# Kernel tuning notes

Hardware: AMD Instinct MI355X
Metric: run time of the kernel (lower is better)

Reference implementation:

```python
import jax, jax.numpy as jnp
import numpy as np

N = 32          # agents_num
IN_DIM = 16     # node feature dim (excluding 2 pos cols)
HID = 128
HEADS = 4
OUT = 5
DUEL_H = 256
RADIUS = 0.3
LATENT = HID + HID * HEADS * 2  # 1152
BS = 128


def _lin(k, i, o):
    s = 1.0 / np.sqrt(i)
    return jax.random.uniform(k, (i, o), minval=-s, maxval=s, dtype=jnp.float32)


def setup_inputs() -> dict:
    key = jax.random.key(0)
    ks = jax.random.split(key, 16)
    pos = jax.random.uniform(ks[0], (BS, N, 2))
    feats = jax.random.normal(ks[1], (BS, N, IN_DIM))
    aidx = jax.random.randint(ks[2], (BS,), 0, N).astype(jnp.float32)
    node = jnp.concatenate([pos, feats], axis=-1).reshape(BS, N * (2 + IN_DIM))
    obs = jnp.concatenate([node, aidx[:, None]], axis=1)  # (BS, N*(2+IN_DIM)+1)
    return {
        "obs": obs,
        "enc_w1": _lin(ks[3], IN_DIM, HID), "enc_b1": jnp.zeros((HID,)),
        "enc_w2": _lin(ks[4], HID, HID), "enc_b2": jnp.zeros((HID,)),
        "wl1": _lin(ks[5], HID, HEADS * HID), "wr1": _lin(ks[6], HID, HEADS * HID),
        "att1": jax.random.normal(ks[7], (HEADS, HID)) * 0.1, "bias1": jnp.zeros((HEADS * HID,)),
        "wl2": _lin(ks[8], HID * HEADS, HEADS * HID), "wr2": _lin(ks[9], HID * HEADS, HEADS * HID),
        "att2": jax.random.normal(ks[10], (HEADS, HID)) * 0.1, "bias2": jnp.zeros((HEADS * HID,)),
        "q_w1": _lin(ks[11], LATENT, DUEL_H), "q_b1": jnp.zeros((DUEL_H,)),
        "q_w2": _lin(ks[12], DUEL_H, OUT), "q_b2": jnp.zeros((OUT,)),
        "v_w1": _lin(ks[13], LATENT, DUEL_H), "v_b1": jnp.zeros((DUEL_H,)),
        "v_w2": _lin(ks[14], DUEL_H, 1), "v_b2": jnp.zeros((1,)),
    }


def _gatv2(x, adj, wl, wr, att, bias):
    # Dense-masked GATv2 (PyG semantics: lin_l on source j, lin_r on target i,
    # leaky_relu(x_i + x_j) . att, softmax over neighbors j, aggregate lin_l(x_j)).
    bs, n, _ = x.shape
    gl = (x @ wl).reshape(bs, n, HEADS, HID)  # source transform
    gr = (x @ wr).reshape(bs, n, HEADS, HID)  # target transform
    e = jax.nn.leaky_relu(gr[:, :, None] + gl[:, None, :], 0.2)  # [b, i, j, h, c]
    logits = jnp.einsum('bijhc,hc->bijh', e, att)
    logits = jnp.where(adj[..., None], logits, -jnp.inf)  # diag always True (self loops)
    alpha = jax.nn.softmax(logits, axis=2)
    out = jnp.einsum('bijh,bjhc->bihc', alpha, gl).reshape(bs, n, HEADS * HID)
    return out + bias


def reference(obs, enc_w1, enc_b1, enc_w2, enc_b2,
              wl1, wr1, att1, bias1, wl2, wr2, att2, bias2,
              q_w1, q_b1, q_w2, q_b2, v_w1, v_b1, v_w2, v_b2):
    bs = obs.shape[0]
    node = obs[:, :-1].reshape(bs, N, 2 + IN_DIM)
    pos, feats = node[..., :2], node[..., 2:]
    aidx = jnp.clip(obs[:, -1], 0, N - 1).astype(jnp.int32)

    # radius_graph (per-graph, loop=False) + GATv2 add_self_loops => diag True
    d2 = jnp.sum((pos[:, :, None] - pos[:, None, :]) ** 2, axis=-1)  # [bs, N, N]
    adj = (d2 < RADIUS ** 2) | jnp.eye(N, dtype=bool)

    # encoder MLP then ReLU (as in forward)
    h = jax.nn.relu(feats @ enc_w1 + enc_b1)
    x = jax.nn.relu(h @ enc_w2 + enc_b2)  # [bs, N, HID]

    b = jnp.arange(bs)
    x1 = x[b, aidx]  # [bs, HID]

    x = jax.nn.relu(_gatv2(x, adj, wl1, wr1, att1, bias1))  # [bs, N, HID*HEADS]
    x2 = x[b, aidx]

    x = jax.nn.relu(_gatv2(x, adj, wl2, wr2, att2, bias2))
    x3 = x[b, aidx]

    x_cat = jnp.concatenate([x1, x2, x3], axis=1)  # [bs, LATENT]

    q = jax.nn.relu(x_cat @ q_w1 + q_b1) @ q_w2 + q_b2  # [bs, OUT]
    v = jax.nn.relu(x_cat @ v_w1 + v_b1) @ v_w2 + v_b2  # [bs, 1]
    return q - q.mean(axis=1, keepdims=True) + v
```

## Files before the change

### kernel.cpp

```cpp
#include <hip/hip_runtime.h>
#include <hip/hip_bf16.h>

typedef unsigned int uint_t;
typedef unsigned short ushort_t;
typedef __attribute__((ext_vector_type(8))) short short8;
typedef __attribute__((ext_vector_type(4))) float floatx4;

__device__ __forceinline__ float4 fma4(float4 a, float s, float4 w){
  a.x += s*w.x; a.y += s*w.y; a.z += s*w.z; a.w += s*w.w; return a;
}
__device__ __forceinline__ float4 relu4(float4 a){
  return make_float4(fmaxf(a.x,0.f),fmaxf(a.y,0.f),fmaxf(a.z,0.f),fmaxf(a.w,0.f));
}
__device__ __forceinline__ unsigned bf16rne(float f){
  unsigned u = __float_as_uint(f);
  return (u + 0x7fffu + ((u>>16)&1u)) >> 16;
}
__device__ __forceinline__ uint_t packbf(float f){
  unsigned hb = bf16rne(f);
  float hf = __uint_as_float(hb<<16);
  unsigned lb = bf16rne(f - hf);
  return (hb<<16) | lb;
}
__device__ __forceinline__ uint4 pack4(float4 v){
  uint4 u; u.x=packbf(v.x); u.y=packbf(v.y); u.z=packbf(v.z); u.w=packbf(v.w); return u;
}
__device__ __forceinline__ float unpk(uint_t u){
  return __uint_as_float(u & 0xffff0000u) + __uint_as_float(u<<16);
}
#define UNPACK8(u0,u1,hi,lo) \
  hi[0]=(short)(u0.x>>16); lo[0]=(short)u0.x; \
  hi[1]=(short)(u0.y>>16); lo[1]=(short)u0.y; \
  hi[2]=(short)(u0.z>>16); lo[2]=(short)u0.z; \
  hi[3]=(short)(u0.w>>16); lo[3]=(short)u0.w; \
  hi[4]=(short)(u1.x>>16); lo[4]=(short)u1.x; \
  hi[5]=(short)(u1.y>>16); lo[5]=(short)u1.y; \
  hi[6]=(short)(u1.z>>16); lo[6]=(short)u1.z; \
  hi[7]=(short)(u1.w>>16); lo[7]=(short)u1.w;


template<int NKC>
__device__ __forceinline__ void hgemm_body(
    const uint_t* __restrict__ xcatpk,
    const ushort_t* __restrict__ qw1Thi, const ushort_t* __restrict__ qw1Tlo,
    const ushort_t* __restrict__ vw1Thi, const ushort_t* __restrict__ vw1Tlo,
    float* __restrict__ part, int ks, int ct, int t, int k0c, int slot0)
{
  const int w = t>>6, lane = t&63, m = lane&15, quad = lane>>4;
  const ushort_t* Bhi = (ct<4) ? qw1Thi : vw1Thi;
  const int cbl = (ct<4) ? ct*64 : (ct-4)*64;
  const int cbg = (ct<4) ? ct*64 : 256 + (ct-4)*64;
  const int kb = k0c + ks*NKC;
  const uint_t* ap = xcatpk + (size_t)w*18432 + m*32 + quad*8 + (size_t)kb*512;
  const ushort_t* bp0 = Bhi + (size_t)((cbl>>4)+0)*18432 + m*32 + quad*8 + (size_t)kb*512;
  const ushort_t* bp1 = Bhi + (size_t)((cbl>>4)+1)*18432 + m*32 + quad*8 + (size_t)kb*512;
  const ushort_t* bp2 = Bhi + (size_t)((cbl>>4)+2)*18432 + m*32 + quad*8 + (size_t)kb*512;
  const ushort_t* bp3 = Bhi + (size_t)((cbl>>4)+3)*18432 + m*32 + quad*8 + (size_t)kb*512;
  const size_t lod = (size_t)(qw1Tlo - qw1Thi);
  floatx4 acc[4];
  #pragma unroll
  for (int i=0;i<4;i++) acc[i] = (floatx4){0.f,0.f,0.f,0.f};
  #pragma unroll
  for (int kc=0; kc<NKC; kc++){
    const uint4 ua0 = *(const uint4*)(ap);
    const uint4 ua1 = *(const uint4*)(ap+4);
    ap += 512;
    short8 ahi, alo;
    UNPACK8(ua0,ua1,ahi,alo)
    const ushort_t* bps[4] = {bp0, bp1, bp2, bp3};
    #pragma unroll
    for (int nt=0; nt<4; nt++){
      const short8 bh = *(const short8*)(bps[nt] + kc*512);
      const short8 bl = *(const short8*)(bps[nt] + kc*512 + lod);
      acc[nt] = __builtin_amdgcn_mfma_f32_16x16x32_bf16(ahi, bh, acc[nt], 0,0,0);
      acc[nt] = __builtin_amdgcn_mfma_f32_16x16x32_bf16(ahi, bl, acc[nt], 0,0,0);
      acc[nt] = __builtin_amdgcn_mfma_f32_16x16x32_bf16(alo, bh, acc[nt], 0,0,0);
    }
  }
  float* pdst = part + (size_t)(slot0+ks)*65536;
  const int crow0 = w*16 + quad*4;
  #pragma unroll
  for (int nt=0; nt<4; nt++){
    const int col = cbg + nt*16 + m;
    #pragma unroll
    for (int r=0;r<4;r++)
      pdst[(size_t)(crow0 + r)*512 + col] = acc[nt][r];
  }
}

__global__ __launch_bounds__(256) void prep_kernel(
    const float* __restrict__ obs,
    const float* __restrict__ enc_w1, const float* __restrict__ enc_b1,
    const float* __restrict__ enc_w2, const float* __restrict__ enc_b2,
    const float* __restrict__ wl1, const float* __restrict__ wr1,
    ushort_t* __restrict__ wl1Thi, ushort_t* __restrict__ wl1Tlo,
    ushort_t* __restrict__ wr1Thi, ushort_t* __restrict__ wr1Tlo,
    uint_t* __restrict__ xpk, uint_t* __restrict__ xcatpk,
    unsigned* __restrict__ adjw, int* __restrict__ aiw)
{
  const int t = threadIdx.x, bid = blockIdx.x;
  if (bid >= 512){
    __shared__ float sm[32][33];
    const int cw = bid - 512;
    const float* in; ushort_t* ohi; ushort_t* olo; int tt;
    const int K = 128, N = 512;
    if (cw < 64){ in=wl1; ohi=wl1Thi; olo=wl1Tlo; tt=cw; }
    else        { in=wr1; ohi=wr1Thi; olo=wr1Tlo; tt=cw-64; }
    const int ktiles = K>>5;
    const int kt = tt % ktiles, nt = tt / ktiles;
    const int r = t>>5, c = t&31;
    #pragma unroll
    for (int i=0;i<4;i++)
      sm[r+i*8][c] = in[(size_t)(kt*32 + r + i*8)*N + nt*32 + c];
    __syncthreads();
    #pragma unroll
    for (int i=0;i<4;i++){
      const int nl = r + i*8;
      const int n  = nt*32 + nl;
      const float f = sm[c][nl];
      const unsigned hb = bf16rne(f);
      const float hf = __uint_as_float(hb<<16);
      const unsigned lb = bf16rne(f - hf);
      const size_t off = (size_t)(n>>4)*(16*K) + (size_t)kt*512 + (size_t)(n&15)*32 + c;
      ohi[off] = (ushort_t)hb;
      olo[off] = (ushort_t)lb;
    }
    return;
  }
  __shared__ float s_pos[64];
  __shared__ float s_feats[128];
  __shared__ __align__(16) float s_h[8*132];
  __shared__ int s_ai;
  const int s = bid & 127, g = bid >> 7;
  const float* ob = obs + s*577;

  if (t==0){
    float a = ob[576];
    a = fminf(fmaxf(a, 0.f), 31.f);
    s_ai = (int)a;
    if (g==0) aiw[s] = (int)a;
  }
  if (t < 128){ const int n=t>>4, f=t&15; s_feats[t] = ob[(g*8+n)*18+2+f]; }
  if (g==0 && t>=128 && t<192){ const int u=t-128; s_pos[u] = ob[(u>>1)*18 + (u&1)]; }
  __syncthreads();

  if (g==0 && t < 32){
    const float px = s_pos[2*t], py = s_pos[2*t+1];
    const float R2 = 0.09f;
    unsigned mm = 0u;
    for (int j=0;j<32;j++){
      const float dx = __fsub_rn(px, s_pos[2*j]), dy = __fsub_rn(py, s_pos[2*j+1]);
      const float d2 = __fadd_rn(__fmul_rn(dx,dx), __fmul_rn(dy,dy));
      if (d2 <= R2 || j==t) mm |= (1u<<j);
    }
    adjw[s*32+t] = mm;
  }

  const int n = t>>5, c0 = (t&31)*4;
  {
    float4 a = *(const float4*)(enc_b1+c0);
    #pragma unroll
    for (int f=0; f<16; f++)
      a = fma4(a, s_feats[n*16+f], *(const float4*)(enc_w1 + f*128 + c0));
    *(float4*)&s_h[n*132+c0] = relu4(a);
  }
  __syncthreads();
  {
    float4 a = *(const float4*)(enc_b2+c0);
    for (int k=0;k<128;k+=4){
      const float4 hv = *(const float4*)&s_h[n*132+k];
      a = fma4(a, hv.x, *(const float4*)(enc_w2 + (k+0)*128 + c0));
      a = fma4(a, hv.y, *(const float4*)(enc_w2 + (k+1)*128 + c0));
      a = fma4(a, hv.z, *(const float4*)(enc_w2 + (k+2)*128 + c0));
      a = fma4(a, hv.w, *(const float4*)(enc_w2 + (k+3)*128 + c0));
    }
    a = relu4(a);
    const uint4 p = pack4(a);
    const int i = g*8 + n;
    uint_t* xp = xpk + (size_t)(s*2 + (i>>4))*2048 + (c0>>5)*512 + (i&15)*32 + (c0&31);
    *(uint4*)xp = p;
    if (i == s_ai){
      uint_t* xc = xcatpk + (size_t)(s>>4)*18432 + (c0>>5)*512 + (s&15)*32 + (c0&31);
      *(uint4*)xc = p;
    }
  }
}

__global__ __launch_bounds__(512) void pa1_kernel(
    const uint_t* __restrict__ xpk,
    const ushort_t* __restrict__ wl1Thi, const ushort_t* __restrict__ wl1Tlo,
    const ushort_t* __restrict__ wr1Thi, const ushort_t* __restrict__ wr1Tlo,
    const float* __restrict__ att, const float* __restrict__ bias,
    const unsigned* __restrict__ adjw, const int* __restrict__ aiw,
    const float* __restrict__ wl2, const float* __restrict__ q_w1,
    const float* __restrict__ v_w1, const float* __restrict__ wr2,
    ushort_t* __restrict__ wl2Thi, ushort_t* __restrict__ wl2Tlo,
    ushort_t* __restrict__ qw1Thi, ushort_t* __restrict__ qw1Tlo,
    ushort_t* __restrict__ vw1Thi, ushort_t* __restrict__ vw1Tlo,
    ushort_t* __restrict__ wr2Thi, ushort_t* __restrict__ wr2Tlo,
    uint_t* __restrict__ x2pk, uint_t* __restrict__ xcatpk)
{
  __shared__ __align__(16) float s_gl[32*132];
  __shared__ __align__(16) float s_gr[32*132];
  __shared__ __align__(16) float s_att[128];
  __shared__ __align__(16) float s_b[128];
  __shared__ float s_lg[32*33];
  __shared__ unsigned s_adj[32];
  const int t = threadIdx.x, bid = blockIdx.x;

  if (bid >= 512){
    const int cw = bid - 512;
    const float* in; ushort_t* ohi; ushort_t* olo; int K, N, tt;
    if (cw < 256)      { in=wl2;  ohi=wl2Thi; olo=wl2Tlo; K=512;  N=512; tt=cw; }
    else if (cw < 544) { in=q_w1; ohi=qw1Thi; olo=qw1Tlo; K=1152; N=256; tt=cw-256; }
    else if (cw < 832) { in=v_w1; ohi=vw1Thi; olo=vw1Tlo; K=1152; N=256; tt=cw-544; }
    else               { in=wr2;  ohi=wr2Thi; olo=wr2Tlo; K=512;  N=512; tt=cw-832; }
    const int ktiles = K>>5;
    const int kt = tt % ktiles, nt = tt / ktiles;
    const int r = t>>5, c = t&31;
    #pragma unroll
    for (int i=0;i<2;i++)
      s_gl[(r+i*16)*33 + c] = in[(size_t)(kt*32 + r + i*16)*N + nt*32 + c];
    __syncthreads();
    #pragma unroll
    for (int i=0;i<2;i++){
      const int nl = r + i*16;
      const int n  = nt*32 + nl;
      const float f = s_gl[c*33 + nl];
      const unsigned hb = bf16rne(f);
      const float hf = __uint_as_float(hb<<16);
      const unsigned lb = bf16rne(f - hf);
      const size_t off = (size_t)(n>>4)*(16*K) + (size_t)kt*512 + (size_t)(n&15)*32 + c;
      ohi[off] = (ushort_t)hb;
      olo[off] = (ushort_t)lb;
    }
    return;
  }

  const int s = bid & 127, h = bid >> 7;
  const int w = t>>6, lane = t&63, m = lane&15, quad = lane>>4;
  const int mat = w>>2, cpair = w&3;

  if (t < 128){ s_att[t] = att[h*128 + t]; s_b[t] = bias[h*128 + t]; }
  if (t >= 224 && t < 256) s_adj[t-224] = adjw[s*32 + (t-224)];
  const int ai = aiw[s];

  const ushort_t* Bhi = (mat==0) ? wl1Thi : wr1Thi;
  const ushort_t* Blo = (mat==0) ? wl1Tlo : wr1Tlo;
  const int nbase = h*8 + cpair*2;
  const uint_t* a0p = xpk + (size_t)(s*2+0)*2048 + m*32 + quad*8;
  const uint_t* a1p = xpk + (size_t)(s*2+1)*2048 + m*32 + quad*8;
  const ushort_t* bp0 = Bhi + (size_t)(nbase+0)*2048 + m*32 + quad*8;
  const ushort_t* bp1 = Bhi + (size_t)(nbase+1)*2048 + m*32 + quad*8;
  const size_t lod = (size_t)(Blo - Bhi);
  floatx4 acc[2][2];
  #pragma unroll
  for (int i=0;i<2;i++)
    #pragma unroll
    for (int j=0;j<2;j++) acc[i][j] = (floatx4){0.f,0.f,0.f,0.f};

  #pragma unroll
  for (int kc=0; kc<4; kc++){
    const uint4 u00 = *(const uint4*)(a0p + kc*512);
    const uint4 u01 = *(const uint4*)(a0p + kc*512 + 4);
    const uint4 u10 = *(const uint4*)(a1p + kc*512);
    const uint4 u11 = *(const uint4*)(a1p + kc*512 + 4);
    short8 ahi0, alo0, ahi1, alo1;
    UNPACK8(u00,u01,ahi0,alo0)
    UNPACK8(u10,u11,ahi1,alo1)
    const ushort_t* bps[2] = {bp0, bp1};
    #pragma unroll
    for (int nt=0; nt<2; nt++){
      const short8 bh = *(const short8*)(bps[nt] + kc*512);
      const short8 bl = *(const short8*)(bps[nt] + kc*512 + lod);
      acc[0][nt] = __builtin_amdgcn_mfma_f32_16x16x32_bf16(ahi0, bh, acc[0][nt], 0,0,0);
      acc[0][nt] = __builtin_amdgcn_mfma_f32_16x16x32_bf16(ahi0, bl, acc[0][nt], 0,0,0);
      acc[0][nt] = __builtin_amdgcn_mfma_f32_16x16x32_bf16(alo0, bh, acc[0][nt], 0,0,0);
      acc[1][nt] = __builtin_amdgcn_mfma_f32_16x16x32_bf16(ahi1, bh, acc[1][nt], 0,0,0);
      acc[1][nt] = __builtin_amdgcn_mfma_f32_16x16x32_bf16(ahi1, bl, acc[1][nt], 0,0,0);
      acc[1][nt] = __builtin_amdgcn_mfma_f32_16x16x32_bf16(alo1, bh, acc[1][nt], 0,0,0);
    }
  }
  {
    float* dst = mat ? s_gr : s_gl;
    const int colbase = cpair*32;
    #pragma unroll
    for (int nt=0; nt<2; nt++){
      const int col = colbase + nt*16 + m;
      #pragma unroll
      for (int r=0;r<4;r++){
        dst[(quad*4+r)*132 + col]      = acc[0][nt][r];
        dst[(16+quad*4+r)*132 + col]   = acc[1][nt][r];
      }
    }
  }
  __syncthreads();

  {
    const int i = t>>4, jb = t&15;
    float lacc[2] = {0.f,0.f};
    for (int c=0;c<128;c+=4){
      const float4 g = *(const float4*)&s_gr[i*132+c];
      const float4 a = *(const float4*)&s_att[c];
      #pragma unroll
      for (int mm=0;mm<2;mm++){
        const float4 gj = *(const float4*)&s_gl[(jb+16*mm)*132 + c];
        float ex = g.x+gj.x; ex = fmaxf(ex, 0.2f*ex);
        float ey = g.y+gj.y; ey = fmaxf(ey, 0.2f*ey);
        float ez = g.z+gj.z; ez = fmaxf(ez, 0.2f*ez);
        float ew = g.w+gj.w; ew = fmaxf(ew, 0.2f*ew);
        lacc[mm] += ex*a.x + ey*a.y + ez*a.z + ew*a.w;
      }
    }
    s_lg[i*33 + jb]      = lacc[0];
    s_lg[i*33 + jb + 16] = lacc[1];
  }
  __syncthreads();

  #pragma unroll
  for (int rnd=0; rnd<2; rnd++){
    const int i = rnd*16 + (t>>5), j = t&31;
    const float lg = s_lg[i*33+j];
    const bool ok = (s_adj[i]>>j)&1u;
    float v = ok ? lg : -3.0e38f;
    #pragma unroll
    for (int d_=16; d_; d_>>=1) v = fmaxf(v, __shfl_xor(v, d_, 32));
    const float e = ok ? __expf(lg - v) : 0.f;
    float sum = e;
    #pragma unroll
    for (int d_=16; d_; d_>>=1) sum += __shfl_xor(sum, d_, 32);
    s_lg[i*33+j] = e / sum;
  }
  __syncthreads();

  {
    const int i = t>>4, c0 = (t&15)*8;
    float4 o0 = make_float4(0.f,0.f,0.f,0.f), o1 = o0;
    for (int j=0;j<32;j++){
      const float al = s_lg[i*33+j];
      o0 = fma4(o0, al, *(const float4*)&s_gl[j*132 + c0]);
      o1 = fma4(o1, al, *(const float4*)&s_gl[j*132 + c0 + 4]);
    }
    const float4 b0 = *(const float4*)&s_b[c0];
    const float4 b1 = *(const float4*)&s_b[c0+4];
    o0 = relu4(make_float4(o0.x+b0.x, o0.y+b0.y, o0.z+b0.z, o0.w+b0.w));
    o1 = relu4(make_float4(o1.x+b1.x, o1.y+b1.y, o1.z+b1.z, o1.w+b1.w));
    const uint4 p0 = pack4(o0), p1 = pack4(o1);
    const int kb = h*128 + c0;
    uint_t* xp = x2pk + (size_t)(s*2 + (i>>4))*8192 + (kb>>5)*512 + (i&15)*32 + (kb&31);
    *(uint4*)&xp[0] = p0;
    *(uint4*)&xp[4] = p1;
    if (i == ai){
      const int kk = 128 + kb;
      uint_t* tp = xcatpk + (size_t)(s>>4)*18432 + (kk>>5)*512 + (s&15)*32 + (kk&31);
      *(uint4*)&tp[0] = p0;
      *(uint4*)&tp[4] = p1;
    }
  }
}

__global__ __launch_bounds__(512) void gr2_kernel(
    const uint_t* __restrict__ xcatpk,
    const ushort_t* __restrict__ wr2Thi, const ushort_t* __restrict__ wr2Tlo,
    const ushort_t* __restrict__ qw1Thi, const ushort_t* __restrict__ qw1Tlo,
    const ushort_t* __restrict__ vw1Thi, const ushort_t* __restrict__ vw1Tlo,
    float* __restrict__ hpart, float* __restrict__ GR)
{
  const int t = threadIdx.x, bid = blockIdx.x;
  if (bid >= 32){
    const int hk = bid - 32;
    hgemm_body<5>(xcatpk, qw1Thi, qw1Tlo, vw1Thi, vw1Tlo, hpart, hk>>3, hk&7, t, 0, 0);
    return;
  }
  const int w = t>>6, lane = t&63, m = lane&15, quad = lane>>4;
  const int rt = w;
  const int ctl = bid;
  const uint_t* ap = xcatpk + (size_t)rt*18432 + m*32 + quad*8 + (size_t)4*512;
  const ushort_t* bp = wr2Thi + (size_t)ctl*8192 + m*32 + quad*8;
  const size_t lod = (size_t)(wr2Tlo - wr2Thi);
  floatx4 acc = (floatx4){0.f,0.f,0.f,0.f};
  #pragma unroll 4
  for (int kc=0; kc<16; kc++){
    const uint4 ua0 = *(const uint4*)(ap + kc*512);
    const uint4 ua1 = *(const uint4*)(ap + kc*512 + 4);
    short8 ahi, alo;
    UNPACK8(ua0,ua1,ahi,alo)
    const short8 bh = *(const short8*)(bp + kc*512);
    const short8 bl = *(const short8*)(bp + kc*512 + lod);
    acc = __builtin_amdgcn_mfma_f32_16x16x32_bf16(ahi, bh, acc, 0,0,0);
    acc = __builtin_amdgcn_mfma_f32_16x16x32_bf16(ahi, bl, acc, 0,0,0);
    acc = __builtin_amdgcn_mfma_f32_16x16x32_bf16(alo, bh, acc, 0,0,0);
  }
  const int row0 = rt*16 + quad*4, col = ctl*16 + m;
  #pragma unroll
  for (int r=0;r<4;r++)
    GR[(size_t)(row0 + r)*512 + col] = acc[r];
}

__global__ __launch_bounds__(512) void pa2_kernel(
    const uint_t* __restrict__ x2pk,
    const ushort_t* __restrict__ wl2Thi, const ushort_t* __restrict__ wl2Tlo,
    const float* __restrict__ GR,
    const float* __restrict__ att2, const float* __restrict__ bias2,
    const unsigned* __restrict__ adjw, const int* __restrict__ aiw,
    uint_t* __restrict__ xcatpk)
{
  __shared__ __align__(16) float s_gl[32*132];
  __shared__ __align__(16) float s_p2[128];
  __shared__ __align__(16) float s_at[128];
  __shared__ __align__(16) float s_bb[128];
  __shared__ float s_lg[32];
  __shared__ float s_al[32];
  const int t = threadIdx.x, bid = blockIdx.x;
  const int s = bid & 127, h = bid >> 7;
  const int w = t>>6, lane = t&63, m = lane&15, quad = lane>>4;
  const int ai = aiw[s];
  const unsigned arow = adjw[s*32+ai];

  if (t < 128){
    s_p2[t] = GR[(size_t)s*512 + h*128 + t];
    s_at[t] = att2[h*128+t];
    s_bb[t] = bias2[h*128+t];
  }

  const uint_t* a0p = x2pk + (size_t)(s*2+0)*8192 + m*32 + quad*8;
  const uint_t* a1p = x2pk + (size_t)(s*2+1)*8192 + m*32 + quad*8;
  const ushort_t* bq = wl2Thi + (size_t)(h*8 + w)*8192 + m*32 + quad*8;
  const size_t lod = (size_t)(wl2Tlo - wl2Thi);
  floatx4 acc0 = (floatx4){0.f,0.f,0.f,0.f}, acc1 = acc0;
  #pragma unroll 4
  for (int kc=0; kc<16; kc++){
    const uint4 u00 = *(const uint4*)(a0p + kc*512);
    const uint4 u01 = *(const uint4*)(a0p + kc*512 + 4);
    const uint4 u10 = *(const uint4*)(a1p + kc*512);
    const uint4 u11 = *(const uint4*)(a1p + kc*512 + 4);
    short8 ahi0, alo0, ahi1, alo1;
    UNPACK8(u00,u01,ahi0,alo0)
    UNPACK8(u10,u11,ahi1,alo1)
    const short8 bh = *(const short8*)(bq + kc*512);
    const short8 bl = *(const short8*)(bq + kc*512 + lod);
    acc0 = __builtin_amdgcn_mfma_f32_16x16x32_bf16(ahi0, bh, acc0, 0,0,0);
    acc0 = __builtin_amdgcn_mfma_f32_16x16x32_bf16(ahi0, bl, acc0, 0,0,0);
    acc0 = __builtin_amdgcn_mfma_f32_16x16x32_bf16(alo0, bh, acc0, 0,0,0);
    acc1 = __builtin_amdgcn_mfma_f32_16x16x32_bf16(ahi1, bh, acc1, 0,0,0);
    acc1 = __builtin_amdgcn_mfma_f32_16x16x32_bf16(ahi1, bl, acc1, 0,0,0);
    acc1 = __builtin_amdgcn_mfma_f32_16x16x32_bf16(alo1, bh, acc1, 0,0,0);
  }
  {
    const int col = w*16 + m;
    #pragma unroll
    for (int r=0;r<4;r++){
      s_gl[(quad*4+r)*132 + col]    = acc0[r];
      s_gl[(16+quad*4+r)*132 + col] = acc1[r];
    }
  }
  __syncthreads();

  if (t < 256){
    const int j = t>>3, pq = t&7;
    float sum = 0.f;
    #pragma unroll
    for (int q=0;q<4;q++){
      const int c = pq*16 + q*4;
      const float4 g = *(const float4*)&s_gl[j*132 + c];
      const float4 r = *(const float4*)&s_p2[c];
      const float4 a = *(const float4*)&s_at[c];
      float e0 = r.x+g.x; e0 = fmaxf(e0, 0.2f*e0);
      float e1 = r.y+g.y; e1 = fmaxf(e1, 0.2f*e1);
      float e2 = r.z+g.z; e2 = fmaxf(e2, 0.2f*e2);
      float e3 = r.w+g.w; e3 = fmaxf(e3, 0.2f*e3);
      sum += e0*a.x + e1*a.y + e2*a.z + e3*a.w;
    }
    sum += __shfl_xor(sum,1,64);
    sum += __shfl_xor(sum,2,64);
    sum += __shfl_xor(sum,4,64);
    if (pq==0) s_lg[j] = sum;
  }
  __syncthreads();
  if (t < 32){
    const float lg = s_lg[t];
    const bool ok = (arow>>t)&1u;
    float v = ok ? lg : -3.0e38f;
    #pragma unroll
    for (int d_=16; d_; d_>>=1) v = fmaxf(v, __shfl_xor(v, d_, 32));
    const float e = ok ? __expf(lg - v) : 0.f;
    float sm = e;
    #pragma unroll
    for (int d_=16; d_; d_>>=1) sm += __shfl_xor(sm, d_, 32);
    s_al[t] = e / sm;
  }
  __syncthreads();
  if (t < 128){
    float acc2 = 0.f;
    #pragma unroll 8
    for (int j=0;j<32;j++) acc2 += s_al[j] * s_gl[j*132 + t];
    const float x3v = fmaxf(acc2 + s_bb[t], 0.f);
    const int kk = 640 + h*128 + t;
    xcatpk[(size_t)(s>>4)*18432 + (kk>>5)*512 + (s&15)*32 + (kk&31)] = packbf(x3v);
  }
}

__global__ __launch_bounds__(512) void x3g_kernel(
    const uint_t* __restrict__ xcatpk,
    const ushort_t* __restrict__ qw1Thi, const ushort_t* __restrict__ qw1Tlo,
    const ushort_t* __restrict__ vw1Thi, const ushort_t* __restrict__ vw1Tlo,
    float* __restrict__ hpart)
{
  const int t = threadIdx.x, bid = blockIdx.x;
  hgemm_body<4>(xcatpk, qw1Thi, qw1Tlo, vw1Thi, vw1Tlo, hpart, bid>>3, bid&7, t, 20, 4);
}

__global__ __launch_bounds__(256) void hepi_kernel(
    const float* __restrict__ hpart,
    const float* __restrict__ q_b1, const float* __restrict__ q_w2, const float* __restrict__ q_b2,
    const float* __restrict__ v_b1, const float* __restrict__ v_w2, const float* __restrict__ v_b2,
    float* __restrict__ out)
{
  __shared__ float s_p[4*6];
  const int t = threadIdx.x, s = blockIdx.x;
  float hq = q_b1[t], hv = v_b1[t];
  #pragma unroll
  for (int ks=0; ks<8; ks++){
    hq += hpart[(size_t)ks*65536 + (size_t)s*512 + t];
    hv += hpart[(size_t)ks*65536 + (size_t)s*512 + 256 + t];
  }
  hq = fmaxf(hq, 0.f);
  hv = fmaxf(hv, 0.f);
  float p[6];
  #pragma unroll
  for (int o=0;o<5;o++) p[o] = hq * q_w2[t*5+o];
  p[5] = hv * v_w2[t];
  #pragma unroll
  for (int d_=32; d_; d_>>=1){
    #pragma unroll
    for (int o=0;o<6;o++) p[o] += __shfl_xor(p[o], d_, 64);
  }
  const int w = t>>6, lane = t&63;
  if (lane==0){
    #pragma unroll
    for (int o=0;o<6;o++) s_p[w*6+o] = p[o];
  }
  __syncthreads();
  if (t < 6) s_p[t] = s_p[t] + s_p[6+t] + s_p[12+t] + s_p[18+t];
  __syncthreads();
  if (t < 5){
    const float q0 = s_p[0]+q_b2[0], q1 = s_p[1]+q_b2[1], q2 = s_p[2]+q_b2[2],
                q3 = s_p[3]+q_b2[3], q4 = s_p[4]+q_b2[4];
    const float mean = (q0+q1+q2+q3+q4) / 5.0f;
    const float v = s_p[5] + v_b2[0];
    const float qt = (t==0?q0:t==1?q1:t==2?q2:t==3?q3:q4);
    out[s*5+t] = qt - mean + v;
  }
}

extern "C" void kernel_launch(void* const* d_in, const int* in_sizes, int n_in,
                              void* d_out, int out_size, void* d_ws, size_t ws_size,
                              hipStream_t stream) {
  (void)n_in; (void)out_size; (void)ws_size;
  const float* obs    = (const float*)d_in[0];
  const float* enc_w1 = (const float*)d_in[1];
  const float* enc_b1 = (const float*)d_in[2];
  const float* enc_w2 = (const float*)d_in[3];
  const float* enc_b2 = (const float*)d_in[4];
  const float* wl1    = (const float*)d_in[5];
  const float* wr1    = (const float*)d_in[6];
  const float* att1   = (const float*)d_in[7];
  const float* bias1  = (const float*)d_in[8];
  const float* wl2    = (const float*)d_in[9];
  const float* wr2    = (const float*)d_in[10];
  const float* att2   = (const float*)d_in[11];
  const float* bias2  = (const float*)d_in[12];
  const float* q_w1   = (const float*)d_in[13];
  const float* q_b1   = (const float*)d_in[14];
  const float* q_w2   = (const float*)d_in[15];
  const float* q_b2   = (const float*)d_in[16];
  const float* v_w1   = (const float*)d_in[17];
  const float* v_b1   = (const float*)d_in[18];
  const float* v_w2   = (const float*)d_in[19];
  const float* v_b2   = (const float*)d_in[20];

  char* ws = (char*)d_ws;
  uint_t*   x_pk    = (uint_t*)  (ws + 0);
  float*    hpart   = (float*)   (ws + 0);
  uint_t*   xcat_pk = (uint_t*)  (ws + 2097152);
  unsigned* adjw    = (unsigned*)(ws + 2686976);
  int*      aiw     = (int*)     (ws + 2703360);
  uint_t*   x2_pk   = (uint_t*)  (ws + 2703872);
  ushort_t* wl1Thi  = (ushort_t*)(ws + 11092480);
  ushort_t* wl1Tlo  = (ushort_t*)(ws + 11223552);
  ushort_t* wr1Thi  = (ushort_t*)(ws + 11354624);
  ushort_t* wr1Tlo  = (ushort_t*)(ws + 11485696);
  ushort_t* wl2Thi  = (ushort_t*)(ws + 11616768);
  ushort_t* wl2Tlo  = (ushort_t*)(ws + 12141056);
  ushort_t* qw1Thi  = (ushort_t*)(ws + 12665344);
  ushort_t* qw1Tlo  = (ushort_t*)(ws + 13255168);
  ushort_t* vw1Thi  = (ushort_t*)(ws + 13844992);
  ushort_t* vw1Tlo  = (ushort_t*)(ws + 14434816);
  ushort_t* wr2Thi  = (ushort_t*)(ws + 15024640);
  ushort_t* wr2Tlo  = (ushort_t*)(ws + 15548928);
  float*    GR      = (float*)   (ws + 16073216);

  const int bs = in_sizes[0] / 577;
  (void)bs;

  prep_kernel<<<512 + 128, 256, 0, stream>>>(obs, enc_w1, enc_b1, enc_w2, enc_b2,
      wl1, wr1, wl1Thi, wl1Tlo, wr1Thi, wr1Tlo,
      x_pk, xcat_pk, adjw, aiw);

  pa1_kernel<<<512 + 1088, 512, 0, stream>>>(x_pk, wl1Thi, wl1Tlo, wr1Thi, wr1Tlo,
      att1, bias1, adjw, aiw,
      wl2, q_w1, v_w1, wr2,
      wl2Thi, wl2Tlo, qw1Thi, qw1Tlo, vw1Thi, vw1Tlo, wr2Thi, wr2Tlo,
      x2_pk, xcat_pk);

  gr2_kernel<<<64, 512, 0, stream>>>(xcat_pk, wr2Thi, wr2Tlo,
      qw1Thi, qw1Tlo, vw1Thi, vw1Tlo, hpart, GR);

  pa2_kernel<<<512, 512, 0, stream>>>(x2_pk, wl2Thi, wl2Tlo, GR,
      att2, bias2, adjw, aiw, xcat_pk);

  x3g_kernel<<<32, 512, 0, stream>>>(xcat_pk, qw1Thi, qw1Tlo, vw1Thi, vw1Tlo, hpart);

  hepi_kernel<<<128, 256, 0, stream>>>(hpart, q_b1, q_w2, q_b2, v_b1, v_w2, v_b2,
                                       (float*)d_out);
}
```

Before: 197.0 us.

## Fuse second GAT layer and dueling head into one per-sample tail kernel

Replaces the gr2, pa2, x3g and hepi kernels with a single tail kernel, one block per sample. Each block gathers the agent rows, computes the wr2 target projection and the q/v first layers as plain fp32 GEMVs reading the original weights, and loops over the four heads for layer-2 attention. This drops three launches, the bf16 hi/lo transposes of q_w1, v_w1 and wr2, and the partial-sum round trips through global memory. In exchange, only 128 blocks run and the heads are processed one after another. Each block also re-reads several MB of fp32 weights with scalar FMA loops instead of MFMA, which could leave the tail latency- and bandwidth-bound.

```diff
diff --git a/kernel.cpp b/kernel.cpp
--- a/kernel.cpp
+++ b/kernel.cpp
@@ -39,55 +39,6 @@
   hi[7]=(short)(u1.w>>16); lo[7]=(short)u1.w;
 
 
-template<int NKC>
-__device__ __forceinline__ void hgemm_body(
-    const uint_t* __restrict__ xcatpk,
-    const ushort_t* __restrict__ qw1Thi, const ushort_t* __restrict__ qw1Tlo,
-    const ushort_t* __restrict__ vw1Thi, const ushort_t* __restrict__ vw1Tlo,
-    float* __restrict__ part, int ks, int ct, int t, int k0c, int slot0)
-{
-  const int w = t>>6, lane = t&63, m = lane&15, quad = lane>>4;
-  const ushort_t* Bhi = (ct<4) ? qw1Thi : vw1Thi;
-  const int cbl = (ct<4) ? ct*64 : (ct-4)*64;
-  const int cbg = (ct<4) ? ct*64 : 256 + (ct-4)*64;
-  const int kb = k0c + ks*NKC;
-  const uint_t* ap = xcatpk + (size_t)w*18432 + m*32 + quad*8 + (size_t)kb*512;
-  const ushort_t* bp0 = Bhi + (size_t)((cbl>>4)+0)*18432 + m*32 + quad*8 + (size_t)kb*512;
-  const ushort_t* bp1 = Bhi + (size_t)((cbl>>4)+1)*18432 + m*32 + quad*8 + (size_t)kb*512;
-  const ushort_t* bp2 = Bhi + (size_t)((cbl>>4)+2)*18432 + m*32 + quad*8 + (size_t)kb*512;
-  const ushort_t* bp3 = Bhi + (size_t)((cbl>>4)+3)*18432 + m*32 + quad*8 + (size_t)kb*512;
-  const size_t lod = (size_t)(qw1Tlo - qw1Thi);
-  floatx4 acc[4];
-  #pragma unroll
-  for (int i=0;i<4;i++) acc[i] = (floatx4){0.f,0.f,0.f,0.f};
-  #pragma unroll
-  for (int kc=0; kc<NKC; kc++){
-    const uint4 ua0 = *(const uint4*)(ap);
-    const uint4 ua1 = *(const uint4*)(ap+4);
-    ap += 512;
-    short8 ahi, alo;
-    UNPACK8(ua0,ua1,ahi,alo)
-    const ushort_t* bps[4] = {bp0, bp1, bp2, bp3};
-    #pragma unroll
-    for (int nt=0; nt<4; nt++){
-      const short8 bh = *(const short8*)(bps[nt] + kc*512);
-      const short8 bl = *(const short8*)(bps[nt] + kc*512 + lod);
-      acc[nt] = __builtin_amdgcn_mfma_f32_16x16x32_bf16(ahi, bh, acc[nt], 0,0,0);
-      acc[nt] = __builtin_amdgcn_mfma_f32_16x16x32_bf16(ahi, bl, acc[nt], 0,0,0);
-      acc[nt] = __builtin_amdgcn_mfma_f32_16x16x32_bf16(alo, bh, acc[nt], 0,0,0);
-    }
-  }
-  float* pdst = part + (size_t)(slot0+ks)*65536;
-  const int crow0 = w*16 + quad*4;
-  #pragma unroll
-  for (int nt=0; nt<4; nt++){
-    const int col = cbg + nt*16 + m;
-    #pragma unroll
-    for (int r=0;r<4;r++)
-      pdst[(size_t)(crow0 + r)*512 + col] = acc[nt][r];
-  }
-}
-
 __global__ __launch_bounds__(256) void prep_kernel(
     const float* __restrict__ obs,
     const float* __restrict__ enc_w1, const float* __restrict__ enc_b1,
@@ -95,7 +46,7 @@
     const float* __restrict__ wl1, const float* __restrict__ wr1,
     ushort_t* __restrict__ wl1Thi, ushort_t* __restrict__ wl1Tlo,
     ushort_t* __restrict__ wr1Thi, ushort_t* __restrict__ wr1Tlo,
-    uint_t* __restrict__ xpk, uint_t* __restrict__ xcatpk,
+    uint_t* __restrict__ xpk,
     unsigned* __restrict__ adjw, int* __restrict__ aiw)
 {
   const int t = threadIdx.x, bid = blockIdx.x;
@@ -179,10 +130,6 @@
     const int i = g*8 + n;
     uint_t* xp = xpk + (size_t)(s*2 + (i>>4))*2048 + (c0>>5)*512 + (i&15)*32 + (c0&31);
     *(uint4*)xp = p;
-    if (i == s_ai){
-      uint_t* xc = xcatpk + (size_t)(s>>4)*18432 + (c0>>5)*512 + (s&15)*32 + (c0&31);
-      *(uint4*)xc = p;
-    }
   }
 }
 
@@ -191,14 +138,10 @@
     const ushort_t* __restrict__ wl1Thi, const ushort_t* __restrict__ wl1Tlo,
     const ushort_t* __restrict__ wr1Thi, const ushort_t* __restrict__ wr1Tlo,
     const float* __restrict__ att, const float* __restrict__ bias,
-    const unsigned* __restrict__ adjw, const int* __restrict__ aiw,
-    const float* __restrict__ wl2, const float* __restrict__ q_w1,
-    const float* __restrict__ v_w1, const float* __restrict__ wr2,
+    const unsigned* __restrict__ adjw,
+    const float* __restrict__ wl2,
     ushort_t* __restrict__ wl2Thi, ushort_t* __restrict__ wl2Tlo,
-    ushort_t* __restrict__ qw1Thi, ushort_t* __restrict__ qw1Tlo,
-    ushort_t* __restrict__ vw1Thi, ushort_t* __restrict__ vw1Tlo,
-    ushort_t* __restrict__ wr2Thi, ushort_t* __restrict__ wr2Tlo,
-    uint_t* __restrict__ x2pk, uint_t* __restrict__ xcatpk)
+    uint_t* __restrict__ x2pk)
 {
   __shared__ __align__(16) float s_gl[32*132];
   __shared__ __align__(16) float s_gr[32*132];
@@ -209,18 +152,12 @@
   const int t = threadIdx.x, bid = blockIdx.x;
 
   if (bid >= 512){
-    const int cw = bid - 512;
-    const float* in; ushort_t* ohi; ushort_t* olo; int K, N, tt;
-    if (cw < 256)      { in=wl2;  ohi=wl2Thi; olo=wl2Tlo; K=512;  N=512; tt=cw; }
-    else if (cw < 544) { in=q_w1; ohi=qw1Thi; olo=qw1Tlo; K=1152; N=256; tt=cw-256; }
-    else if (cw < 832) { in=v_w1; ohi=vw1Thi; olo=vw1Tlo; K=1152; N=256; tt=cw-544; }
-    else               { in=wr2;  ohi=wr2Thi; olo=wr2Tlo; K=512;  N=512; tt=cw-832; }
-    const int ktiles = K>>5;
-    const int kt = tt % ktiles, nt = tt / ktiles;
+    const int tt = bid - 512;
+    const int kt = tt & 15, nt = tt >> 4;
     const int r = t>>5, c = t&31;
     #pragma unroll
     for (int i=0;i<2;i++)
-      s_gl[(r+i*16)*33 + c] = in[(size_t)(kt*32 + r + i*16)*N + nt*32 + c];
+      s_gl[(r+i*16)*33 + c] = wl2[(size_t)(kt*32 + r + i*16)*512 + nt*32 + c];
     __syncthreads();
     #pragma unroll
     for (int i=0;i<2;i++){
@@ -230,9 +167,9 @@
       const unsigned hb = bf16rne(f);
       const float hf = __uint_as_float(hb<<16);
       const unsigned lb = bf16rne(f - hf);
-      const size_t off = (size_t)(n>>4)*(16*K) + (size_t)kt*512 + (size_t)(n&15)*32 + c;
-      ohi[off] = (ushort_t)hb;
-      olo[off] = (ushort_t)lb;
+      const size_t off = (size_t)(n>>4)*8192 + (size_t)kt*512 + (size_t)(n&15)*32 + c;
+      wl2Thi[off] = (ushort_t)hb;
+      wl2Tlo[off] = (ushort_t)lb;
     }
     return;
   }
@@ -243,7 +180,6 @@
 
   if (t < 128){ s_att[t] = att[h*128 + t]; s_b[t] = bias[h*128 + t]; }
   if (t >= 224 && t < 256) s_adj[t-224] = adjw[s*32 + (t-224)];
-  const int ai = aiw[s];
 
   const ushort_t* Bhi = (mat==0) ? wl1Thi : wr1Thi;
   const ushort_t* Blo = (mat==0) ? wl1Tlo : wr1Tlo;
@@ -350,204 +286,166 @@
     uint_t* xp = x2pk + (size_t)(s*2 + (i>>4))*8192 + (kb>>5)*512 + (i&15)*32 + (kb&31);
     *(uint4*)&xp[0] = p0;
     *(uint4*)&xp[4] = p1;
-    if (i == ai){
-      const int kk = 128 + kb;
-      uint_t* tp = xcatpk + (size_t)(s>>4)*18432 + (kk>>5)*512 + (s&15)*32 + (kk&31);
-      *(uint4*)&tp[0] = p0;
-      *(uint4*)&tp[4] = p1;
-    }
-  }
-}
-
-__global__ __launch_bounds__(512) void gr2_kernel(
-    const uint_t* __restrict__ xcatpk,
-    const ushort_t* __restrict__ wr2Thi, const ushort_t* __restrict__ wr2Tlo,
-    const ushort_t* __restrict__ qw1Thi, const ushort_t* __restrict__ qw1Tlo,
-    const ushort_t* __restrict__ vw1Thi, const ushort_t* __restrict__ vw1Tlo,
-    float* __restrict__ hpart, float* __restrict__ GR)
-{
-  const int t = threadIdx.x, bid = blockIdx.x;
-  if (bid >= 32){
-    const int hk = bid - 32;
-    hgemm_body<5>(xcatpk, qw1Thi, qw1Tlo, vw1Thi, vw1Tlo, hpart, hk>>3, hk&7, t, 0, 0);
-    return;
-  }
-  const int w = t>>6, lane = t&63, m = lane&15, quad = lane>>4;
-  const int rt = w;
-  const int ctl = bid;
-  const uint_t* ap = xcatpk + (size_t)rt*18432 + m*32 + quad*8 + (size_t)4*512;
-  const ushort_t* bp = wr2Thi + (size_t)ctl*8192 + m*32 + quad*8;
-  const size_t lod = (size_t)(wr2Tlo - wr2Thi);
-  floatx4 acc = (floatx4){0.f,0.f,0.f,0.f};
-  #pragma unroll 4
-  for (int kc=0; kc<16; kc++){
-    const uint4 ua0 = *(const uint4*)(ap + kc*512);
-    const uint4 ua1 = *(const uint4*)(ap + kc*512 + 4);
-    short8 ahi, alo;
-    UNPACK8(ua0,ua1,ahi,alo)
-    const short8 bh = *(const short8*)(bp + kc*512);
-    const short8 bl = *(const short8*)(bp + kc*512 + lod);
-    acc = __builtin_amdgcn_mfma_f32_16x16x32_bf16(ahi, bh, acc, 0,0,0);
-    acc = __builtin_amdgcn_mfma_f32_16x16x32_bf16(ahi, bl, acc, 0,0,0);
-    acc = __builtin_amdgcn_mfma_f32_16x16x32_bf16(alo, bh, acc, 0,0,0);
-  }
-  const int row0 = rt*16 + quad*4, col = ctl*16 + m;
-  #pragma unroll
-  for (int r=0;r<4;r++)
-    GR[(size_t)(row0 + r)*512 + col] = acc[r];
-}
-
-__global__ __launch_bounds__(512) void pa2_kernel(
-    const uint_t* __restrict__ x2pk,
+  }
+}
+
+__global__ __launch_bounds__(512) void tail_kernel(
+    const uint_t* __restrict__ xpk, const uint_t* __restrict__ x2pk,
     const ushort_t* __restrict__ wl2Thi, const ushort_t* __restrict__ wl2Tlo,
-    const float* __restrict__ GR,
+    const float* __restrict__ wr2,
     const float* __restrict__ att2, const float* __restrict__ bias2,
     const unsigned* __restrict__ adjw, const int* __restrict__ aiw,
-    uint_t* __restrict__ xcatpk)
+    const float* __restrict__ q_w1, const float* __restrict__ q_b1,
+    const float* __restrict__ q_w2, const float* __restrict__ q_b2,
+    const float* __restrict__ v_w1, const float* __restrict__ v_b1,
+    const float* __restrict__ v_w2, const float* __restrict__ v_b2,
+    float* __restrict__ out)
 {
   __shared__ __align__(16) float s_gl[32*132];
-  __shared__ __align__(16) float s_p2[128];
+  __shared__ __align__(16) float s_xc[1152];
+  __shared__ __align__(16) float s_p2[512];
   __shared__ __align__(16) float s_at[128];
   __shared__ __align__(16) float s_bb[128];
   __shared__ float s_lg[32];
   __shared__ float s_al[32];
-  const int t = threadIdx.x, bid = blockIdx.x;
-  const int s = bid & 127, h = bid >> 7;
+  __shared__ float s_p6[8*6];
+  const int t = threadIdx.x, s = blockIdx.x;
   const int w = t>>6, lane = t&63, m = lane&15, quad = lane>>4;
   const int ai = aiw[s];
   const unsigned arow = adjw[s*32+ai];
 
-  if (t < 128){
-    s_p2[t] = GR[(size_t)s*512 + h*128 + t];
-    s_at[t] = att2[h*128+t];
-    s_bb[t] = bias2[h*128+t];
-  }
-
-  const uint_t* a0p = x2pk + (size_t)(s*2+0)*8192 + m*32 + quad*8;
-  const uint_t* a1p = x2pk + (size_t)(s*2+1)*8192 + m*32 + quad*8;
-  const ushort_t* bq = wl2Thi + (size_t)(h*8 + w)*8192 + m*32 + quad*8;
+  if (t < 128)
+    s_xc[t] = unpk(xpk[(size_t)(s*2 + (ai>>4))*2048 + (t>>5)*512 + (ai&15)*32 + (t&31)]);
+  s_xc[128+t] = unpk(x2pk[(size_t)(s*2 + (ai>>4))*8192 + (t>>5)*512 + (ai&15)*32 + (t&31)]);
+  __syncthreads();
+
+  {
+    float acc = 0.f;
+    #pragma unroll 8
+    for (int k=0;k<512;k++) acc += s_xc[128+k] * wr2[(size_t)k*512 + t];
+    s_p2[t] = acc;
+  }
+
   const size_t lod = (size_t)(wl2Tlo - wl2Thi);
-  floatx4 acc0 = (floatx4){0.f,0.f,0.f,0.f}, acc1 = acc0;
-  #pragma unroll 4
-  for (int kc=0; kc<16; kc++){
-    const uint4 u00 = *(const uint4*)(a0p + kc*512);
-    const uint4 u01 = *(const uint4*)(a0p + kc*512 + 4);
-    const uint4 u10 = *(const uint4*)(a1p + kc*512);
-    const uint4 u11 = *(const uint4*)(a1p + kc*512 + 4);
-    short8 ahi0, alo0, ahi1, alo1;
-    UNPACK8(u00,u01,ahi0,alo0)
-    UNPACK8(u10,u11,ahi1,alo1)
-    const short8 bh = *(const short8*)(bq + kc*512);
-    const short8 bl = *(const short8*)(bq + kc*512 + lod);
-    acc0 = __builtin_amdgcn_mfma_f32_16x16x32_bf16(ahi0, bh, acc0, 0,0,0);
-    acc0 = __builtin_amdgcn_mfma_f32_16x16x32_bf16(ahi0, bl, acc0, 0,0,0);
-    acc0 = __builtin_amdgcn_mfma_f32_16x16x32_bf16(alo0, bh, acc0, 0,0,0);
-    acc1 = __builtin_amdgcn_mfma_f32_16x16x32_bf16(ahi1, bh, acc1, 0,0,0);
-    acc1 = __builtin_amdgcn_mfma_f32_16x16x32_bf16(ahi1, bl, acc1, 0,0,0);
-    acc1 = __builtin_amdgcn_mfma_f32_16x16x32_bf16(alo1, bh, acc1, 0,0,0);
-  }
-  {
-    const int col = w*16 + m;
-    #pragma unroll
-    for (int r=0;r<4;r++){
-      s_gl[(quad*4+r)*132 + col]    = acc0[r];
-      s_gl[(16+quad*4+r)*132 + col] = acc1[r];
-    }
-  }
-  __syncthreads();
-
-  if (t < 256){
-    const int j = t>>3, pq = t&7;
-    float sum = 0.f;
-    #pragma unroll
-    for (int q=0;q<4;q++){
-      const int c = pq*16 + q*4;
-      const float4 g = *(const float4*)&s_gl[j*132 + c];
-      const float4 r = *(const float4*)&s_p2[c];
-      const float4 a = *(const float4*)&s_at[c];
-      float e0 = r.x+g.x; e0 = fmaxf(e0, 0.2f*e0);
-      float e1 = r.y+g.y; e1 = fmaxf(e1, 0.2f*e1);
-      float e2 = r.z+g.z; e2 = fmaxf(e2, 0.2f*e2);
-      float e3 = r.w+g.w; e3 = fmaxf(e3, 0.2f*e3);
-      sum += e0*a.x + e1*a.y + e2*a.z + e3*a.w;
-    }
-    sum += __shfl_xor(sum,1,64);
-    sum += __shfl_xor(sum,2,64);
-    sum += __shfl_xor(sum,4,64);
-    if (pq==0) s_lg[j] = sum;
-  }
-  __syncthreads();
-  if (t < 32){
-    const float lg = s_lg[t];
-    const bool ok = (arow>>t)&1u;
-    float v = ok ? lg : -3.0e38f;
-    #pragma unroll
-    for (int d_=16; d_; d_>>=1) v = fmaxf(v, __shfl_xor(v, d_, 32));
-    const float e = ok ? __expf(lg - v) : 0.f;
-    float sm = e;
-    #pragma unroll
-    for (int d_=16; d_; d_>>=1) sm += __shfl_xor(sm, d_, 32);
-    s_al[t] = e / sm;
-  }
-  __syncthreads();
-  if (t < 128){
-    float acc2 = 0.f;
+  for (int h=0; h<4; h++){
+    const uint_t* a0p = x2pk + (size_t)(s*2+0)*8192 + m*32 + quad*8;
+    const uint_t* a1p = x2pk + (size_t)(s*2+1)*8192 + m*32 + quad*8;
+    const ushort_t* bq = wl2Thi + (size_t)(h*8 + w)*8192 + m*32 + quad*8;
+    floatx4 acc0 = (floatx4){0.f,0.f,0.f,0.f}, acc1 = acc0;
+    #pragma unroll 4
+    for (int kc=0; kc<16; kc++){
+      const uint4 u00 = *(const uint4*)(a0p + kc*512);
+      const uint4 u01 = *(const uint4*)(a0p + kc*512 + 4);
+      const uint4 u10 = *(const uint4*)(a1p + kc*512);
+      const uint4 u11 = *(const uint4*)(a1p + kc*512 + 4);
+      short8 ahi0, alo0, ahi1, alo1;
+      UNPACK8(u00,u01,ahi0,alo0)
+      UNPACK8(u10,u11,ahi1,alo1)
+      const short8 bh = *(const short8*)(bq + kc*512);
+      const short8 bl = *(const short8*)(bq + kc*512 + lod);
+      acc0 = __builtin_amdgcn_mfma_f32_16x16x32_bf16(ahi0, bh, acc0, 0,0,0);
+      acc0 = __builtin_amdgcn_mfma_f32_16x16x32_bf16(ahi0, bl, acc0, 0,0,0);
+      acc0 = __builtin_amdgcn_mfma_f32_16x16x32_bf16(alo0, bh, acc0, 0,0,0);
+      acc1 = __builtin_amdgcn_mfma_f32_16x16x32_bf16(ahi1, bh, acc1, 0,0,0);
+      acc1 = __builtin_amdgcn_mfma_f32_16x16x32_bf16(ahi1, bl, acc1, 0,0,0);
+      acc1 = __builtin_amdgcn_mfma_f32_16x16x32_bf16(alo1, bh, acc1, 0,0,0);
+    }
+    if (t < 128){ s_at[t] = att2[h*128+t]; s_bb[t] = bias2[h*128+t]; }
+    {
+      const int col = w*16 + m;
+      #pragma unroll
+      for (int r=0;r<4;r++){
+        s_gl[(quad*4+r)*132 + col]    = acc0[r];
+        s_gl[(16+quad*4+r)*132 + col] = acc1[r];
+      }
+    }
+    __syncthreads();
+
+    if (t < 256){
+      const int j = t>>3, pq = t&7;
+      float sum = 0.f;
+      #pragma unroll
+      for (int q=0;q<4;q++){
+        const int c = pq*16 + q*4;
+        const float4 g = *(const float4*)&s_gl[j*132 + c];
+        const float4 r = *(const float4*)&s_p2[h*128 + c];
+        const float4 a = *(const float4*)&s_at[c];
+        float e0 = r.x+g.x; e0 = fmaxf(e0, 0.2f*e0);
+        float e1 = r.y+g.y; e1 = fmaxf(e1, 0.2f*e1);
+        float e2 = r.z+g.z; e2 = fmaxf(e2, 0.2f*e2);
+        float e3 = r.w+g.w; e3 = fmaxf(e3, 0.2f*e3);
+        sum += e0*a.x + e1*a.y + e2*a.z + e3*a.w;
+      }
+      sum += __shfl_xor(sum,1,64);
+      sum += __shfl_xor(sum,2,64);
+      sum += __shfl_xor(sum,4,64);
+      if (pq==0) s_lg[j] = sum;
+    }
+    __syncthreads();
+    if (t < 32){
+      const float lg = s_lg[t];
+      const bool ok = (arow>>t)&1u;
+      float v = ok ? lg : -3.0e38f;
+      #pragma unroll
+      for (int d_=16; d_; d_>>=1) v = fmaxf(v, __shfl_xor(v, d_, 32));
+      const float e = ok ? __expf(lg - v) : 0.f;
+      float sm = e;
+      #pragma unroll
+      for (int d_=16; d_; d_>>=1) sm += __shfl_xor(sm, d_, 32);
+      s_al[t] = e / sm;
+    }
+    __syncthreads();
+    if (t < 128){
+      float acc2 = 0.f;
+      #pragma unroll 8
+      for (int j=0;j<32;j++) acc2 += s_al[j] * s_gl[j*132 + t];
+      s_xc[640 + h*128 + t] = fmaxf(acc2 + s_bb[t], 0.f);
+    }
+    __syncthreads();
+  }
+
+  float val;
+  {
+    const float* W = (t<256) ? q_w1 : v_w1;
+    const float* B = (t<256) ? q_b1 : v_b1;
+    const int col = t & 255;
+    float acc = 0.f;
     #pragma unroll 8
-    for (int j=0;j<32;j++) acc2 += s_al[j] * s_gl[j*132 + t];
-    const float x3v = fmaxf(acc2 + s_bb[t], 0.f);
-    const int kk = 640 + h*128 + t;
-    xcatpk[(size_t)(s>>4)*18432 + (kk>>5)*512 + (s&15)*32 + (kk&31)] = packbf(x3v);
-  }
-}
-
-__global__ __launch_bounds__(512) void x3g_kernel(
-    const uint_t* __restrict__ xcatpk,
-    const ushort_t* __restrict__ qw1Thi, const ushort_t* __restrict__ qw1Tlo,
-    const ushort_t* __restrict__ vw1Thi, const ushort_t* __restrict__ vw1Tlo,
-    float* __restrict__ hpart)
-{
-  const int t = threadIdx.x, bid = blockIdx.x;
-  hgemm_body<4>(xcatpk, qw1Thi, qw1Tlo, vw1Thi, vw1Tlo, hpart, bid>>3, bid&7, t, 20, 4);
-}
-
-__global__ __launch_bounds__(256) void hepi_kernel(
-    const float* __restrict__ hpart,
-    const float* __restrict__ q_b1, const float* __restrict__ q_w2, const float* __restrict__ q_b2,
-    const float* __restrict__ v_b1, const float* __restrict__ v_w2, const float* __restrict__ v_b2,
-    float* __restrict__ out)
-{
-  __shared__ float s_p[4*6];
-  const int t = threadIdx.x, s = blockIdx.x;
-  float hq = q_b1[t], hv = v_b1[t];
-  #pragma unroll
-  for (int ks=0; ks<8; ks++){
-    hq += hpart[(size_t)ks*65536 + (size_t)s*512 + t];
-    hv += hpart[(size_t)ks*65536 + (size_t)s*512 + 256 + t];
-  }
-  hq = fmaxf(hq, 0.f);
-  hv = fmaxf(hv, 0.f);
+    for (int k=0;k<1152;k++) acc += s_xc[k] * W[(size_t)k*256 + col];
+    val = fmaxf(acc + B[col], 0.f);
+  }
+
   float p[6];
   #pragma unroll
-  for (int o=0;o<5;o++) p[o] = hq * q_w2[t*5+o];
-  p[5] = hv * v_w2[t];
+  for (int o=0;o<6;o++) p[o] = 0.f;
+  if (t < 256){
+    #pragma unroll
+    for (int o=0;o<5;o++) p[o] = val * q_w2[t*5+o];
+  } else {
+    p[5] = val * v_w2[t-256];
+  }
   #pragma unroll
   for (int d_=32; d_; d_>>=1){
     #pragma unroll
     for (int o=0;o<6;o++) p[o] += __shfl_xor(p[o], d_, 64);
   }
-  const int w = t>>6, lane = t&63;
   if (lane==0){
     #pragma unroll
-    for (int o=0;o<6;o++) s_p[w*6+o] = p[o];
-  }
-  __syncthreads();
-  if (t < 6) s_p[t] = s_p[t] + s_p[6+t] + s_p[12+t] + s_p[18+t];
+    for (int o=0;o<6;o++) s_p6[w*6+o] = p[o];
+  }
+  __syncthreads();
+  if (t < 6){
+    float v = 0.f;
+    #pragma unroll
+    for (int ww=0; ww<8; ww++) v += s_p6[ww*6 + t];
+    s_p6[t] = v;
+  }
   __syncthreads();
   if (t < 5){
-    const float q0 = s_p[0]+q_b2[0], q1 = s_p[1]+q_b2[1], q2 = s_p[2]+q_b2[2],
-                q3 = s_p[3]+q_b2[3], q4 = s_p[4]+q_b2[4];
+    const float q0 = s_p6[0]+q_b2[0], q1 = s_p6[1]+q_b2[1], q2 = s_p6[2]+q_b2[2],
+                q3 = s_p6[3]+q_b2[3], q4 = s_p6[4]+q_b2[4];
     const float mean = (q0+q1+q2+q3+q4) / 5.0f;
-    const float v = s_p[5] + v_b2[0];
+    const float v = s_p6[5] + v_b2[0];
     const float qt = (t==0?q0:t==1?q1:t==2?q2:t==3?q3:q4);
     out[s*5+t] = qt - mean + v;
   }
@@ -581,46 +479,26 @@
 
   char* ws = (char*)d_ws;
   uint_t*   x_pk    = (uint_t*)  (ws + 0);
-  float*    hpart   = (float*)   (ws + 0);
-  uint_t*   xcat_pk = (uint_t*)  (ws + 2097152);
-  unsigned* adjw    = (unsigned*)(ws + 2686976);
-  int*      aiw     = (int*)     (ws + 2703360);
-  uint_t*   x2_pk   = (uint_t*)  (ws + 2703872);
-  ushort_t* wl1Thi  = (ushort_t*)(ws + 11092480);
-  ushort_t* wl1Tlo  = (ushort_t*)(ws + 11223552);
-  ushort_t* wr1Thi  = (ushort_t*)(ws + 11354624);
-  ushort_t* wr1Tlo  = (ushort_t*)(ws + 11485696);
-  ushort_t* wl2Thi  = (ushort_t*)(ws + 11616768);
-  ushort_t* wl2Tlo  = (ushort_t*)(ws + 12141056);
-  ushort_t* qw1Thi  = (ushort_t*)(ws + 12665344);
-  ushort_t* qw1Tlo  = (ushort_t*)(ws + 13255168);
-  ushort_t* vw1Thi  = (ushort_t*)(ws + 13844992);
-  ushort_t* vw1Tlo  = (ushort_t*)(ws + 14434816);
-  ushort_t* wr2Thi  = (ushort_t*)(ws + 15024640);
-  ushort_t* wr2Tlo  = (ushort_t*)(ws + 15548928);
-  float*    GR      = (float*)   (ws + 16073216);
-
-  const int bs = in_sizes[0] / 577;
-  (void)bs;
+  unsigned* adjw    = (unsigned*)(ws + 2097152);
+  int*      aiw     = (int*)     (ws + 2113536);
+  uint_t*   x2_pk   = (uint_t*)  (ws + 2114048);
+  ushort_t* wl1Thi  = (ushort_t*)(ws + 10502656);
+  ushort_t* wl1Tlo  = (ushort_t*)(ws + 10633728);
+  ushort_t* wr1Thi  = (ushort_t*)(ws + 10764800);
+  ushort_t* wr1Tlo  = (ushort_t*)(ws + 10895872);
+  ushort_t* wl2Thi  = (ushort_t*)(ws + 11026944);
+  ushort_t* wl2Tlo  = (ushort_t*)(ws + 11551232);
 
   prep_kernel<<<512 + 128, 256, 0, stream>>>(obs, enc_w1, enc_b1, enc_w2, enc_b2,
       wl1, wr1, wl1Thi, wl1Tlo, wr1Thi, wr1Tlo,
-      x_pk, xcat_pk, adjw, aiw);
-
-  pa1_kernel<<<512 + 1088, 512, 0, stream>>>(x_pk, wl1Thi, wl1Tlo, wr1Thi, wr1Tlo,
-      att1, bias1, adjw, aiw,
-      wl2, q_w1, v_w1, wr2,
-      wl2Thi, wl2Tlo, qw1Thi, qw1Tlo, vw1Thi, vw1Tlo, wr2Thi, wr2Tlo,
-      x2_pk, xcat_pk);
-
-  gr2_kernel<<<64, 512, 0, stream>>>(xcat_pk, wr2Thi, wr2Tlo,
-      qw1Thi, qw1Tlo, vw1Thi, vw1Tlo, hpart, GR);
-
-  pa2_kernel<<<512, 512, 0, stream>>>(x2_pk, wl2Thi, wl2Tlo, GR,
-      att2, bias2, adjw, aiw, xcat_pk);
-
-  x3g_kernel<<<32, 512, 0, stream>>>(xcat_pk, qw1Thi, qw1Tlo, vw1Thi, vw1Tlo, hpart);
-
-  hepi_kernel<<<128, 256, 0, stream>>>(hpart, q_b1, q_w2, q_b2, v_b1, v_w2, v_b2,
-                                       (float*)d_out);
-}
+      x_pk, adjw, aiw);
+
+  pa1_kernel<<<512 + 256, 512, 0, stream>>>(x_pk, wl1Thi, wl1Tlo, wr1Thi, wr1Tlo,
+      att1, bias1, adjw,
+      wl2, wl2Thi, wl2Tlo, x2_pk);
+
+  tail_kernel<<<128, 512, 0, stream>>>(x_pk, x2_pk, wl2Thi, wl2Tlo, wr2,
+      att2, bias2, adjw, aiw,
+      q_w1, q_b1, q_w2, q_b2, v_w1, v_b1, v_w2, v_b2,
+      (float*)d_out);
+}
```

Result: slower. 275.1 us (+39.6%).
